# Kernel tuning notes

Measured on AMD Instinct MI355X. Metric: run time of the kernel, lower is better.

Reference implementation:

```python
import jax, jax.numpy as jnp
import numpy as np

B, L, D = 2, 2048, 2048
H, KV, HD = 16, 8, 128
EPS = 1e-5
ROPE_BASE = 10000.0
SCALING_ALPHA = 1.0
SCALE = HD ** -0.5


def setup_inputs() -> dict:
    key = jax.random.key(0)
    ks = jax.random.split(key, 5)
    s = 0.02  # weight init scale
    return {
        "x": jax.random.normal(ks[0], (B, L, D), jnp.float32),
        "wq": jax.random.normal(ks[1], (D, H * HD), jnp.float32) * s,
        "wk": jax.random.normal(ks[2], (D, KV * HD), jnp.float32) * s,
        "wv": jax.random.normal(ks[3], (D, KV * HD), jnp.float32) * s,
        "wo": jax.random.normal(ks[4], (H * HD, D), jnp.float32) * s,
        "qn_w": jnp.ones((HD,), jnp.float32),
        "kn_w": jnp.ones((HD,), jnp.float32),
    }


def _rope(t):
    # t: [B, h, L, HD]. DynamicNTKAlpha base scaling (alpha=1 -> no-op).
    base = ROPE_BASE * SCALING_ALPHA ** (HD / (HD - 2))
    # NOTE: source uses base**(+i/d) (no negative exponent) -- kept faithful.
    freqs = base ** (jnp.arange(0, HD, 2, dtype=jnp.float32) / HD)  # [HD/2]
    pos = jnp.arange(t.shape[-2], dtype=jnp.float32)                # [L]
    angles = pos[:, None] * freqs[None, :]                          # [L, HD/2]
    cos, sin = jnp.cos(angles), jnp.sin(angles)
    x1, x2 = t[..., : HD // 2], t[..., HD // 2 :]
    return jnp.concatenate([x1 * cos - x2 * sin, x2 * cos + x1 * sin], axis=-1)


def _rmsnorm(t, w):
    return t * jax.lax.rsqrt(jnp.mean(t * t, axis=-1, keepdims=True) + EPS) * w


def reference(x, wq, wk, wv, wo, qn_w, kn_w):
    b, l, _ = x.shape
    q = (x @ wq).reshape(b, l, H, HD).transpose(0, 2, 1, 3)   # [B,H,L,HD]
    k = (x @ wk).reshape(b, l, KV, HD).transpose(0, 2, 1, 3)  # [B,KV,L,HD]
    v = (x @ wv).reshape(b, l, KV, HD).transpose(0, 2, 1, 3)
    q = _rmsnorm(_rope(q), qn_w)
    k = _rmsnorm(_rope(k), kn_w)
    # GQA: expand KV heads to match query heads
    rep = H // KV
    k = jnp.repeat(k, rep, axis=1)  # [B,H,L,HD]
    v = jnp.repeat(v, rep, axis=1)
    scores = jnp.einsum("bhqd,bhkd->bhqk", q, k) * SCALE
    probs = jax.nn.softmax(scores, axis=-1)
    out = jnp.einsum("bhqk,bhkd->bhqd", probs, v)             # [B,H,L,HD]
    out = out.transpose(0, 2, 1, 3).reshape(b, l, H * HD)
    return out @ wo
```

## Files before the change

### kernel.cpp

```cpp
#include <hip/hip_runtime.h>
#include <math.h>

#define BB 2
#define LL 2048
#define DD 2048
#define HH 16
#define KVH 8
#define HDIM 128
#define SCALE_F 0.08838834764831845f
#define EPS_F 1e-5f
#define LOG2E 1.4426950408889634f
#define SMAX_F 17.0f
#define QKVW 4096

typedef unsigned short u16;
typedef __attribute__((ext_vector_type(8))) short short8;
typedef __attribute__((ext_vector_type(4))) float f32x4;
typedef __attribute__((ext_vector_type(16))) float f32x16;

#define MFMA16(a, b, c) __builtin_amdgcn_mfma_f32_16x16x32_bf16((a), (b), (c), 0, 0, 0)
#define MFMA32(a, b, c) __builtin_amdgcn_mfma_f32_32x32x16_bf16((a), (b), (c), 0, 0, 0)

__device__ __forceinline__ float b2f(u16 u) {
    union { unsigned int i; float f; } x;
    x.i = ((unsigned int)u) << 16;
    return x.f;
}
__device__ __forceinline__ u16 f2b(float f) {
    unsigned int x = __float_as_uint(f);
    unsigned int r = x + 0x7FFFu + ((x >> 16) & 1u);
    return (u16)(r >> 16);
}
__device__ __forceinline__ unsigned cvtpk(float lo, float hi) {
    unsigned r;
    asm("v_cvt_pk_bf16_f32 %0, %1, %2" : "=v"(r) : "v"(lo), "v"(hi));
    return r;
}
__device__ __forceinline__ void pl32swap(unsigned &a, unsigned &b) {
    asm("v_permlane32_swap_b32 %0, %1" : "+v"(a), "+v"(b));
}
__device__ __forceinline__ void g2l(const u16* g, u16* l) {
    __builtin_amdgcn_global_load_lds(
        (const __attribute__((address_space(1))) unsigned int*)g,
        (__attribute__((address_space(3))) unsigned int*)l, 16, 0, 0);
}

__global__ __launch_bounds__(256) void prep_kernel(const float* __restrict__ x,
                                                   u16* __restrict__ xb,
                                                   const float* __restrict__ wq,
                                                   const float* __restrict__ wk,
                                                   const float* __restrict__ wv,
                                                   const float* __restrict__ wo,
                                                   u16* __restrict__ wqkvT,
                                                   u16* __restrict__ woT,
                                                   float* __restrict__ ct,
                                                   float* __restrict__ st) {
    __shared__ u16 t[64 * 65];
    const int blk = blockIdx.x, tid = threadIdx.x;
    if (blk < 8192) {
        int i = (blk * 256 + tid) * 4;
        float4 v = *(const float4*)(x + i);
        unsigned int p0 = (unsigned int)f2b(v.x) | ((unsigned int)f2b(v.y) << 16);
        unsigned int p1 = (unsigned int)f2b(v.z) | ((unsigned int)f2b(v.w) << 16);
        uint2 pk; pk.x = p0; pk.y = p1;
        *(uint2*)(xb + i) = pk;
    } else if (blk < 11264) {
        int j = blk - 8192;
        const float* in; u16* out; int C, bx, by;
        if (j < 1024)      { in = wq; out = wqkvT;                      C = 2048; bx = j & 31; by = j >> 5; }
        else if (j < 1536) { j -= 1024; in = wk; out = wqkvT + (size_t)2048 * DD; C = 1024; bx = j & 15; by = j >> 4; }
        else if (j < 2048) { j -= 1536; in = wv; out = wqkvT + (size_t)3072 * DD; C = 1024; bx = j & 15; by = j >> 4; }
        else               { j -= 2048; in = wo; out = woT;                      C = 2048; bx = j & 31; by = j >> 5; }
        int c0 = bx * 64, r0 = by * 64;
#pragma unroll
        for (int i = 0; i < 16; i++) {
            int idx = tid + i * 256;
            int r = idx >> 6, c = idx & 63;
            t[r * 65 + c] = f2b(in[(size_t)(r0 + r) * C + c0 + c]);
        }
        __syncthreads();
#pragma unroll
        for (int i = 0; i < 16; i++) {
            int idx = tid + i * 256;
            int r = idx >> 6, c = idx & 63;
            out[(size_t)(c0 + r) * DD + r0 + c] = t[c * 65 + r];
        }
    } else {
        int i = (blk - 11264) * 256 + tid;
        int pos = i >> 6, d = i & 63;
        float freq = (float)pow(10000.0, (double)d * (1.0 / 64.0));
        float ang = (float)pos * freq;
        double a = (double)ang;
        ct[i] = (float)cos(a);
        st[i] = (float)sin(a);
    }
}

__global__ __launch_bounds__(256) void gemm_qkv(const u16* __restrict__ A,
                                                const u16* __restrict__ Bt,
                                                u16* __restrict__ qkv,
                                                u16* __restrict__ vt,
                                                const float* __restrict__ qw,
                                                const float* __restrict__ kw,
                                                const float* __restrict__ ct,
                                                const float* __restrict__ st) {
    __shared__ __align__(16) u16 SM[17408];
    u16* As = SM;
    u16* Bs = SM + 8192;
    const int K = DD, N = QKVW;
    const int tid = threadIdx.x;
    const int w = tid >> 6, lane = tid & 63;
    const int lm = lane & 15, lq = lane >> 4;
    const int bn0 = blockIdx.x * 128, bm0 = blockIdx.y * 128;
    const int wm = (w >> 1) * 64, wn = (w & 1) * 64;

    f32x4 acc[4][4];
#pragma unroll
    for (int i = 0; i < 4; i++)
#pragma unroll
        for (int j = 0; j < 4; j++) acc[i][j] = (f32x4){0.f, 0.f, 0.f, 0.f};

    const int srow = lane >> 3;
    const int sgr = (lane & 7) ^ (srow & 7);
    const u16* ga = A + (size_t)(bm0 + w * 32 + srow) * K + sgr * 8;
    const u16* gb = Bt + (size_t)(bn0 + w * 32 + srow) * K + sgr * 8;
    u16* lA = &As[(w * 32) * 64];
    u16* lB = &Bs[(w * 32) * 64];

    for (int k0 = 0; k0 < K; k0 += 64) {
        __syncthreads();
#pragma unroll
        for (int ch = 0; ch < 4; ch++)
            g2l(ga + (size_t)(ch * 8) * K + k0, lA + ch * 8 * 64);
#pragma unroll
        for (int ch = 0; ch < 4; ch++)
            g2l(gb + (size_t)(ch * 8) * K + k0, lB + ch * 8 * 64);
        __syncthreads();

#pragma unroll
        for (int sub = 0; sub < 2; sub++) {
            short8 af[4], bf[4];
#pragma unroll
            for (int mt = 0; mt < 4; mt++) {
                int row = wm + mt * 16 + lm;
                af[mt] = *(const short8*)(&As[row * 64 + ((sub * 4 + lq) ^ (lm & 7)) * 8]);
            }
#pragma unroll
            for (int nt = 0; nt < 4; nt++) {
                int row = wn + nt * 16 + lm;
                bf[nt] = *(const short8*)(&Bs[row * 64 + ((sub * 4 + lq) ^ (lm & 7)) * 8]);
            }
#pragma unroll
            for (int mt = 0; mt < 4; mt++)
#pragma unroll
                for (int nt = 0; nt < 4; nt++) acc[mt][nt] = MFMA16(af[mt], bf[nt], acc[mt][nt]);
        }
    }

    __syncthreads();
    u16* T = SM;
#pragma unroll
    for (int mt = 0; mt < 4; mt++)
#pragma unroll
        for (int nt = 0; nt < 4; nt++)
#pragma unroll
            for (int r = 0; r < 4; r++) {
                int row = wm + mt * 16 + lq * 4 + r;
                int col = wn + nt * 16 + lm;
                T[row * 136 + col] = f2b(acc[mt][nt][r]);
            }
    __syncthreads();

    const int bx = blockIdx.x;
    const int row = tid >> 1, h = tid & 1;
    if (bx < 24) {
        const float* wgt = (bx < 16) ? qw : kw;
        const int grow = bm0 + row;
        const int pos = grow & (LL - 1);
        const float* crow = ct + pos * 64 + h * 32;
        const float* srw  = st + pos * 64 + h * 32;
        const u16* t1 = &T[row * 136 + h * 32];
        const u16* t2 = t1 + 64;
        float ss = 0.f;
#pragma unroll
        for (int dd = 0; dd < 32; dd++) {
            float x1 = b2f(t1[dd]), x2 = b2f(t2[dd]);
            float c = crow[dd], s = srw[dd];
            float r1 = x1 * c - x2 * s;
            float r2 = x2 * c + x1 * s;
            ss += r1 * r1 + r2 * r2;
        }
        ss += __shfl_xor(ss, 1, 64);
        float sc = 1.0f / sqrtf(ss * (1.0f / 128.0f) + EPS_F);
        u16* out = qkv + (size_t)grow * QKVW + bx * 128 + h * 32;
#pragma unroll
        for (int dd = 0; dd < 32; dd += 2) {
            float x1a = b2f(t1[dd]),     x2a = b2f(t2[dd]);
            float x1b = b2f(t1[dd + 1]), x2b = b2f(t2[dd + 1]);
            float ca = crow[dd],     sa = srw[dd];
            float cb = crow[dd + 1], sb = srw[dd + 1];
            float r1a = x1a * ca - x2a * sa, r2a = x2a * ca + x1a * sa;
            float r1b = x1b * cb - x2b * sb, r2b = x2b * cb + x1b * sb;
            int d = h * 32 + dd;
            unsigned p1 = (unsigned)f2b(r1a * sc * wgt[d]) |
                          ((unsigned)f2b(r1b * sc * wgt[d + 1]) << 16);
            unsigned p2 = (unsigned)f2b(r2a * sc * wgt[d + 64]) |
                          ((unsigned)f2b(r2b * sc * wgt[d + 65]) << 16);
            *(unsigned*)(out + dd) = p1;
            *(unsigned*)(out + 64 + dd) = p2;
        }
    } else {
        const int g = bx - 24;
        const int b = bm0 >> 11;
        const int d = row;
        u16* dst = vt + ((size_t)(b * KVH + g) * HDIM + d) * LL +
                   (bm0 & (LL - 1)) + h * 64;
        const u16* src = &T[(h * 64) * 136 + d];
#pragma unroll
        for (int j = 0; j < 64; j += 2) {
            unsigned pk = (unsigned)src[j * 136] |
                          ((unsigned)src[(j + 1) * 136] << 16);
            *(unsigned*)(dst + j) = pk;
        }
    }
}

__global__ __launch_bounds__(256) void gemm_bt_o(const u16* __restrict__ A,
                                                 const u16* __restrict__ Bt,
                                                 float* __restrict__ C, int M, int N, int K) {
    __shared__ __align__(16) u16 As[64 * 64];
    __shared__ __align__(16) u16 Bs[128 * 64];
    const int tid = threadIdx.x;
    const int w = tid >> 6, lane = tid & 63;
    const int lm = lane & 15, lq = lane >> 4;
    const int bn0 = blockIdx.x * 128, bm0 = blockIdx.y * 64;
    const int wm = (w >> 1) * 32, wn = (w & 1) * 64;

    f32x4 acc[2][4];
#pragma unroll
    for (int i = 0; i < 2; i++)
#pragma unroll
        for (int j = 0; j < 4; j++) acc[i][j] = (f32x4){0.f, 0.f, 0.f, 0.f};

    const int srow = lane >> 3;
    const int sgr = (lane & 7) ^ (srow & 7);
    const u16* ga = A + (size_t)(bm0 + w * 16 + srow) * K + sgr * 8;
    const u16* gb = Bt + (size_t)(bn0 + w * 32 + srow) * K + sgr * 8;
    u16* lA = &As[(w * 16) * 64];
    u16* lB = &Bs[(w * 32) * 64];

    for (int k0 = 0; k0 < K; k0 += 64) {
        __syncthreads();
#pragma unroll
        for (int ch = 0; ch < 2; ch++)
            g2l(ga + (size_t)(ch * 8) * K + k0, lA + ch * 8 * 64);
#pragma unroll
        for (int ch = 0; ch < 4; ch++)
            g2l(gb + (size_t)(ch * 8) * K + k0, lB + ch * 8 * 64);
        __syncthreads();

#pragma unroll
        for (int sub = 0; sub < 2; sub++) {
            short8 af[2], bf[4];
#pragma unroll
            for (int mt = 0; mt < 2; mt++) {
                int row = wm + mt * 16 + lm;
                af[mt] = *(const short8*)(&As[row * 64 + ((sub * 4 + lq) ^ (lm & 7)) * 8]);
            }
#pragma unroll
            for (int nt = 0; nt < 4; nt++) {
                int row = wn + nt * 16 + lm;
                bf[nt] = *(const short8*)(&Bs[row * 64 + ((sub * 4 + lq) ^ (lm & 7)) * 8]);
            }
#pragma unroll
            for (int mt = 0; mt < 2; mt++)
#pragma unroll
                for (int nt = 0; nt < 4; nt++) acc[mt][nt] = MFMA16(af[mt], bf[nt], acc[mt][nt]);
        }
    }

#pragma unroll
    for (int mt = 0; mt < 2; mt++)
#pragma unroll
        for (int nt = 0; nt < 4; nt++)
#pragma unroll
            for (int r = 0; r < 4; r++) {
                int row = bm0 + wm + mt * 16 + lq * 4 + r;
                int col = bn0 + wn + nt * 16 + lm;
                C[(size_t)row * N + col] = acc[mt][nt][r];
            }
}

__global__ __launch_bounds__(256, 3) void attn_kernel(const u16* __restrict__ qkv,
                                                      const u16* __restrict__ vt,
                                                      u16* __restrict__ ob) {
    __shared__ __align__(16) u16 SM[2 * 64 * 128 + 128 * 64];
    u16* Vt = SM + 2 * 64 * 128;

    const int tid = threadIdx.x, w = tid >> 6, lane = tid & 63;
    const int l31 = lane & 31, lh = lane >> 5;
    const int qh = w & 1, kh = w >> 1;

    const int bid = blockIdx.y * 32 + blockIdx.x;
    const int xcd = bid & 7, idx = bid >> 3;
    const int bh = xcd * 4 + (idx >> 5);
    const int q0 = (idx & 31) * 64;
    const int b = bh >> 4, hd = bh & 15, g = hd >> 1;

    const u16* kbase = qkv + (size_t)b * LL * QKVW + 2048 + g * HDIM;
    const u16* vtbase = vt + (size_t)(b * KVH + g) * HDIM * LL;

    const int krl = lane >> 4, kgl = lane & 15;
    const int vrl = lane >> 3, vgl = lane & 7;

#define STAGEK(tt, bi) do {                                                  \
        _Pragma("unroll")                                                    \
        for (int ch = 0; ch < 4; ch++) {                                     \
            int r_ = w * 16 + ch * 4 + krl;                                  \
            int gc_ = kgl ^ (r_ & 15);                                       \
            g2l(kbase + (size_t)((tt) * 64 + r_) * QKVW + gc_ * 8,           \
                SM + (bi) * 8192 + (w * 16 + ch * 4) * 128);                 \
        }                                                                    \
    } while (0)
#define STAGEV(tt) do {                                                      \
        _Pragma("unroll")                                                    \
        for (int ch = 0; ch < 4; ch++) {                                     \
            int r_ = w * 32 + ch * 8 + vrl;                                  \
            int gc_ = vgl ^ (r_ & 7);                                        \
            g2l(vtbase + (size_t)r_ * LL + (tt) * 64 + gc_ * 8,              \
                Vt + (w * 32 + ch * 8) * 64);                                \
        }                                                                    \
    } while (0)

    const int qrow = q0 + qh * 32 + l31;
    short8 aq[8];
    {
        const u16* qp = qkv + (size_t)(b * LL + qrow) * QKVW + hd * HDIM + lh * 8;
#pragma unroll
        for (int kk = 0; kk < 8; kk++) aq[kk] = *(const short8*)(qp + kk * 16);
    }

    f32x16 o[4];
#pragma unroll
    for (int i = 0; i < 4; i++)
#pragma unroll
        for (int r = 0; r < 16; r++) o[i][r] = 0.f;
    float psum = 0.f;
    const float SC2 = SCALE_F * LOG2E;
    const f32x16 fz = {};

    STAGEK(0, 0);
    asm volatile("s_waitcnt vmcnt(0)" ::: "memory");
    __builtin_amdgcn_s_barrier();

    for (int t = 0; t < LL / 64; t++) {
        const int cur = t & 1;
        const u16* Kc = SM + cur * 8192;
        STAGEV(t);
        STAGEK((t + 1) & (LL / 64 - 1), cur ^ 1);

        const int key = kh * 32 + l31;
        f32x16 s;
        __builtin_amdgcn_s_setprio(1);
        {
            int gg = lh ^ (key & 15);
            short8 kf = *(const short8*)(&Kc[key * 128 + gg * 8]);
            s = MFMA32(kf, aq[0], fz);
        }
#pragma unroll
        for (int kk = 1; kk < 8; kk++) {
            int gg = (kk * 2 + lh) ^ (key & 15);
            short8 kf = *(const short8*)(&Kc[key * 128 + gg * 8]);
            s = MFMA32(kf, aq[kk], s);
        }
        __builtin_amdgcn_s_setprio(0);

        float p[16];
#pragma unroll
        for (int r = 0; r < 16; r++) {
            p[r] = __builtin_amdgcn_exp2f(fmaf(s[r], SC2, -SMAX_F));
            psum += p[r];
        }
        unsigned pw[2][4];
#pragma unroll
        for (int half = 0; half < 2; half++) {
            int qb = half * 8;
            unsigned c0 = cvtpk(p[qb + 0], p[qb + 1]);
            unsigned c1 = cvtpk(p[qb + 2], p[qb + 3]);
            unsigned c2 = cvtpk(p[qb + 4], p[qb + 5]);
            unsigned c3 = cvtpk(p[qb + 6], p[qb + 7]);
            pl32swap(c0, c2);
            pl32swap(c1, c3);
            pw[half][0] = c0; pw[half][1] = c1; pw[half][2] = c2; pw[half][3] = c3;
        }

        asm volatile("s_waitcnt vmcnt(4)" ::: "memory");
        __builtin_amdgcn_s_barrier();

        __builtin_amdgcn_s_setprio(1);
#pragma unroll
        for (int kcl = 0; kcl < 2; kcl++) {
            int kc = kh * 2 + kcl;
            union { unsigned u[4]; short8 s8; } pu;
#pragma unroll
            for (int i = 0; i < 4; i++) pu.u[i] = pw[kcl][i];
#pragma unroll
            for (int dn = 0; dn < 4; dn++) {
                int d = dn * 32 + l31;
                int gv = ((kc * 2 + lh) ^ (d & 7)) * 8;
                short8 bv = *(const short8*)(&Vt[d * 64 + gv]);
                o[dn] = MFMA32(pu.s8, bv, o[dn]);
            }
        }
        __builtin_amdgcn_s_setprio(0);

        asm volatile("s_waitcnt vmcnt(0)" ::: "memory");
        __builtin_amdgcn_s_barrier();
    }
#undef STAGEK
#undef STAGEV

    psum += __shfl_xor(psum, 32, 64);

    __syncthreads();
    float* xo = (float*)SM;
    float* xp = xo + 2 * 64 * 68;
    if (kh == 1) {
        float* dst = xo + (qh * 64 + lane) * 68;
#pragma unroll
        for (int dn = 0; dn < 4; dn++)
#pragma unroll
            for (int r = 0; r < 16; r += 4)
                *(f32x4*)(dst + dn * 16 + r) =
                    (f32x4){o[dn][r], o[dn][r + 1], o[dn][r + 2], o[dn][r + 3]};
        xp[qh * 64 + lane] = psum;
    }
    __syncthreads();
    if (kh == 0) {
        const float* src = xo + (qh * 64 + lane) * 68;
        float inv = 1.0f / (psum + xp[qh * 64 + lane]);
        float invr[16];
#pragma unroll
        for (int r = 0; r < 16; r++) {
            int row = (r & 3) + 8 * (r >> 2) + 4 * lh;
            invr[r] = __shfl(inv, row, 32);
        }
        u16* obase = ob + (size_t)(b * LL + q0 + qh * 32) * (HH * HDIM) + hd * HDIM;
#pragma unroll
        for (int dn = 0; dn < 4; dn++)
#pragma unroll
            for (int r = 0; r < 16; r++) {
                int row = (r & 3) + 8 * (r >> 2) + 4 * lh;
                float v = o[dn][r] + src[dn * 16 + r];
                obase[(size_t)row * (HH * HDIM) + dn * 32 + l31] = f2b(v * invr[r]);
            }
    }
}

extern "C" void kernel_launch(void* const* d_in, const int* in_sizes, int n_in,
                              void* d_out, int out_size, void* d_ws, size_t ws_size,
                              hipStream_t stream) {
    const float* x  = (const float*)d_in[0];
    const float* wq = (const float*)d_in[1];
    const float* wk = (const float*)d_in[2];
    const float* wv = (const float*)d_in[3];
    const float* wo = (const float*)d_in[4];
    const float* qn = (const float*)d_in[5];
    const float* kn = (const float*)d_in[6];

    u16* ws = (u16*)d_ws;
    const size_t SZ_X = (size_t)BB * LL * DD;
    u16* xb    = ws;
    u16* qkv   = xb + SZ_X;
    u16* wqkvT = qkv + (size_t)BB * LL * QKVW;
    u16* woT   = wqkvT + (size_t)QKVW * DD;
    float* ct  = (float*)(woT + (size_t)DD * DD);
    float* st  = ct + (size_t)LL * 64;
    u16* vt    = (u16*)(st + (size_t)LL * 64);
    u16* att = xb;

    prep_kernel<<<dim3(11776), dim3(256), 0, stream>>>(x, xb, wq, wk, wv, wo,
                                                       wqkvT, woT, ct, st);
    gemm_qkv<<<dim3(QKVW / 128, BB * LL / 128), dim3(256), 0, stream>>>(
        xb, wqkvT, qkv, vt, qn, kn, ct, st);
    attn_kernel<<<dim3(LL / 64, BB * HH), dim3(256), 0, stream>>>(qkv, vt, att);
    gemm_bt_o<<<dim3(DD / 128, BB * LL / 64), dim3(256), 0, stream>>>(att, woT, (float*)d_out, BB * LL, DD, DD);
}
```

Baseline: 353.9 us.

## Double-buffer LDS tiles in QKV GEMM to overlap global loads with MFMA

```diff
diff --git a/kernel.cpp b/kernel.cpp
--- a/kernel.cpp
+++ b/kernel.cpp
@@ -104,10 +104,8 @@
                                                 const float* __restrict__ kw,
                                                 const float* __restrict__ ct,
                                                 const float* __restrict__ st) {
-    __shared__ __align__(16) u16 SM[17408];
-    u16* As = SM;
-    u16* Bs = SM + 8192;
-    const int K = DD, N = QKVW;
+    __shared__ __align__(16) u16 SM[2][16384];
+    const int K = DD;
     const int tid = threadIdx.x;
     const int w = tid >> 6, lane = tid & 63;
     const int lm = lane & 15, lq = lane >> 4;
@@ -124,18 +122,27 @@
     const int sgr = (lane & 7) ^ (srow & 7);
     const u16* ga = A + (size_t)(bm0 + w * 32 + srow) * K + sgr * 8;
     const u16* gb = Bt + (size_t)(bn0 + w * 32 + srow) * K + sgr * 8;
-    u16* lA = &As[(w * 32) * 64];
-    u16* lB = &Bs[(w * 32) * 64];
+
+#define GSTAGE(k0s, bi) do {                                                 \
+        u16* lA_ = &SM[bi][(w * 32) * 64];                                   \
+        u16* lB_ = &SM[bi][8192 + (w * 32) * 64];                            \
+        _Pragma("unroll")                                                    \
+        for (int ch = 0; ch < 4; ch++)                                       \
+            g2l(ga + (size_t)(ch * 8) * K + (k0s), lA_ + ch * 8 * 64);       \
+        _Pragma("unroll")                                                    \
+        for (int ch = 0; ch < 4; ch++)                                       \
+            g2l(gb + (size_t)(ch * 8) * K + (k0s), lB_ + ch * 8 * 64);       \
+    } while (0)
+
+    GSTAGE(0, 0);
+    asm volatile("s_waitcnt vmcnt(0)" ::: "memory");
+    __builtin_amdgcn_s_barrier();
 
     for (int k0 = 0; k0 < K; k0 += 64) {
-        __syncthreads();
-#pragma unroll
-        for (int ch = 0; ch < 4; ch++)
-            g2l(ga + (size_t)(ch * 8) * K + k0, lA + ch * 8 * 64);
-#pragma unroll
-        for (int ch = 0; ch < 4; ch++)
-            g2l(gb + (size_t)(ch * 8) * K + k0, lB + ch * 8 * 64);
-        __syncthreads();
+        const int cur = (k0 >> 6) & 1;
+        GSTAGE((k0 + 64) & (K - 1), cur ^ 1);
+        const u16* As = &SM[cur][0];
+        const u16* Bs = &SM[cur][8192];
 
 #pragma unroll
         for (int sub = 0; sub < 2; sub++) {
@@ -155,10 +162,13 @@
 #pragma unroll
                 for (int nt = 0; nt < 4; nt++) acc[mt][nt] = MFMA16(af[mt], bf[nt], acc[mt][nt]);
         }
-    }
-
-    __syncthreads();
-    u16* T = SM;
+
+        asm volatile("s_waitcnt vmcnt(0)" ::: "memory");
+        __builtin_amdgcn_s_barrier();
+    }
+#undef GSTAGE
+
+    u16* T = &SM[0][0];
 #pragma unroll
     for (int mt = 0; mt < 4; mt++)
 #pragma unroll
```

Result: slower. 362.3 us (+2.4%).
